# Kernel tuning notes

Measured on AMD Instinct MI355X. Metric: run time of the kernel, lower is better.

The kernel has to match this reference:

```python
import jax, jax.numpy as jnp
import numpy as np

N, D = 128, 512  # batch, hypercube dim (in_features == n_2d_layers == out_features)

def setup_inputs() -> dict:
    key = jax.random.key(0)
    k1, k2, k3 = jax.random.split(key, 3)
    bound = 1.0 / np.sqrt(D)
    x = jax.random.normal(k1, (N, D, D), dtype=jnp.float32)
    # kaiming_uniform_(a=sqrt(5)) on (in, layers, out) ~ U(-1/sqrt(fan_in), 1/sqrt(fan_in)) scale
    w = jax.random.uniform(k2, (D, D, D), dtype=jnp.float32, minval=-bound, maxval=bound)
    b = jax.random.uniform(k3, (D, D), dtype=jnp.float32, minval=-bound, maxval=bound)
    return {"x": x, "w": w, "b": b}

def reference(x, w, b):
    # Original: (x.expand((L, *x.shape)).movedim(0,-2) * w).sum(-1) + b
    # which reduces to out[n,i,j] = sum_k x[n,i,k] * w[i,j,k] + b[i,j]
    # (w axes: (in_features, n_2d_layers, out_features), all equal D)
    return jnp.einsum('nik,ijk->nij', x, w) + b
```

## Files before the change

kernel.cpp:

```cpp
#include <hip/hip_runtime.h>


#define Dd 512
#define DD (512 * 512)

typedef __attribute__((ext_vector_type(8))) short bf16x8;
typedef __attribute__((ext_vector_type(4))) short bf16x4;
typedef __attribute__((ext_vector_type(4))) float f32x4;

__device__ __forceinline__ short f2bf(float f) {
    unsigned u = __builtin_bit_cast(unsigned, f);
    u += 0x7FFFu + ((u >> 16) & 1u);
    return (short)(u >> 16);
}

__device__ __forceinline__ void glds16(const float* g, float* l) {
    __builtin_amdgcn_global_load_lds(
        (const __attribute__((address_space(1))) void*)g,
        (__attribute__((address_space(3))) void*)l, 16, 0, 0);
}

__global__ __launch_bounds__(512, 4)
void linear3d_kernel(const float* __restrict__ x,
                     const float* __restrict__ w,
                     const float* __restrict__ b,
                     float* __restrict__ out) {
    const int i    = blockIdx.x;
    const int tid  = threadIdx.x;
    const int lane = tid & 63;
    const int wid  = tid >> 6;
    const int row16 = lane & 15;
    const int cg    = lane >> 4;

    __shared__ float f32r[2][8192];
    __shared__ short b16s[8192];

    const float* xi = x + (size_t)i * Dd;
    const float* wi = w + (size_t)i * DD;

    #pragma unroll
    for (int q = 0; q < 4; ++q) { int t = wid * 4 + q;
        glds16(wi + t * 256 + lane * 4, &f32r[0][t * 256]); }
    #pragma unroll
    for (int q = 0; q < 4; ++q) { int t = wid * 4 + q;
        glds16(wi + 8192 + t * 256 + lane * 4, &f32r[1][t * 256]); }

    bf16x8 xf[16];
    for (int r = 0; r < 8; ++r) {
        __syncthreads();
        #pragma unroll
        for (int p = 0; p < 4; ++p) {
            int idx4 = tid + p * 512;
            int row = idx4 >> 7, c4 = idx4 & 127;
            float4 v = *(const float4*)(xi + (size_t)(r * 16 + row) * DD + c4 * 4);
            bf16x4 h = { f2bf(v.x), f2bf(v.y), f2bf(v.z), f2bf(v.w) };
            int byte = (row * 1024 + c4 * 8) ^ ((row & 7) << 4);
            *(bf16x4*)((char*)b16s + byte) = h;
        }
        __syncthreads();
        if (wid == r) {
            #pragma unroll
            for (int s = 0; s < 16; ++s) {
                int byte = (row16 * 1024 + s * 64 + cg * 16) ^ ((row16 & 7) << 4);
                xf[s] = *(const bf16x8*)((const char*)b16s + byte);
            }
        }
    }
    __syncthreads();

#define CVTW(V, q) do {                                                        \
    int row_  = 2 * wid + ((q) >> 1);                                          \
    int byte_ = (row_ * 1024 + ((q) & 1) * 512 + lane * 8) ^ ((row_ & 7) << 4);\
    bf16x4 h_ = { f2bf(V.x), f2bf(V.y), f2bf(V.z), f2bf(V.w) };                \
    *(bf16x4*)((char*)b16s + byte_) = h_;                                      \
} while (0)

    {
        asm volatile("s_waitcnt vmcnt(5)" ::: "memory");
        __builtin_amdgcn_sched_barrier(0);
        float4 v0 = *(const float4*)(&f32r[0][wid * 1024 +   0 + lane * 4]);
        float4 v1 = *(const float4*)(&f32r[0][wid * 1024 + 256 + lane * 4]);
        float4 v2 = *(const float4*)(&f32r[0][wid * 1024 + 512 + lane * 4]);
        float4 v3 = *(const float4*)(&f32r[0][wid * 1024 + 768 + lane * 4]);
        asm volatile("s_waitcnt lgkmcnt(0)" ::: "memory");
        __builtin_amdgcn_sched_barrier(0);
        #pragma unroll
        for (int q = 0; q < 4; ++q) { int t = wid * 4 + q;
            glds16(wi + 2 * 8192 + t * 256 + lane * 4, &f32r[0][t * 256]); }
        CVTW(v0, 0); CVTW(v1, 1); CVTW(v2, 2); CVTW(v3, 3);
    }
    float bias = b[i * Dd + row16];
    asm volatile("s_waitcnt lgkmcnt(0)" ::: "memory");
    __builtin_amdgcn_s_barrier();

#define CHUNK_BODY(c, VMSTR, DO_GLDS, DO_CONV) do {                            \
    f32x4 accA = {0.f, 0.f, 0.f, 0.f}, accB = {0.f, 0.f, 0.f, 0.f};           \
    _Pragma("unroll")                                                          \
    for (int s = 0; s < 16; s += 2) {                                          \
        int byA = (row16 * 1024 + s * 64 + cg * 16) ^ ((row16 & 7) << 4);      \
        int byB = (row16 * 1024 + (s + 1) * 64 + cg * 16) ^ ((row16 & 7) << 4);\
        bf16x8 wfA = *(const bf16x8*)((const char*)b16s + byA);                \
        bf16x8 wfB = *(const bf16x8*)((const char*)b16s + byB);                \
        accA = __builtin_amdgcn_mfma_f32_16x16x32_bf16(xf[s], wfA, accA, 0, 0, 0);     \
        accB = __builtin_amdgcn_mfma_f32_16x16x32_bf16(xf[s + 1], wfB, accB, 0, 0, 0); \
    }                                                                          \
    { int j = (c) * 16 + row16;                                                \
      _Pragma("unroll")                                                        \
      for (int r_ = 0; r_ < 4; ++r_) {                                         \
          int n_ = wid * 16 + cg * 4 + r_;                                     \
          out[(size_t)i * Dd + (size_t)n_ * DD + j] = accA[r_] + accB[r_] + bias; \
      } }                                                                      \
    asm volatile("s_waitcnt lgkmcnt(0)" ::: "memory");                         \
    __builtin_amdgcn_s_barrier();                                              \
    if (DO_CONV) {                                                             \
        const float* fb = &f32r[((c) + 1) & 1][0];                             \
        asm volatile("s_waitcnt " VMSTR ::: "memory");                         \
        __builtin_amdgcn_sched_barrier(0);                                     \
        float4 v0 = *(const float4*)(fb + wid * 1024 +   0 + lane * 4);        \
        float4 v1 = *(const float4*)(fb + wid * 1024 + 256 + lane * 4);        \
        float4 v2 = *(const float4*)(fb + wid * 1024 + 512 + lane * 4);        \
        float4 v3 = *(const float4*)(fb + wid * 1024 + 768 + lane * 4);        \
        asm volatile("s_waitcnt lgkmcnt(0)" ::: "memory");                     \
        __builtin_amdgcn_sched_barrier(0);                                     \
        if (DO_GLDS) {                                                         \
            const float* gs = wi + (size_t)((c) + 3) * 8192;                   \
            float* lb = &f32r[((c) + 1) & 1][0];                               \
            _Pragma("unroll")                                                  \
            for (int q = 0; q < 4; ++q) { int t = wid * 4 + q;                 \
                glds16(gs + t * 256 + lane * 4, lb + t * 256); }               \
        }                                                                      \
        bias = b[i * Dd + ((c) + 1) * 16 + row16];                             \
        CVTW(v0, 0); CVTW(v1, 1); CVTW(v2, 2); CVTW(v3, 3);                    \
        asm volatile("s_waitcnt lgkmcnt(0)" ::: "memory");                     \
        __builtin_amdgcn_s_barrier();                                          \
    }                                                                          \
} while (0)

    CHUNK_BODY(0, "vmcnt(9)", true, true);
    for (int c = 1; c <= 29; ++c)
        CHUNK_BODY(c, "vmcnt(14)", (c + 3 < 32), true);
    CHUNK_BODY(30, "vmcnt(10)", false, true);
    CHUNK_BODY(31, "vmcnt(0)", false, false);

#undef CHUNK_BODY
#undef CVTW
}

extern "C" void kernel_launch(void* const* d_in, const int* in_sizes, int n_in,
                              void* d_out, int out_size, void* d_ws, size_t ws_size,
                              hipStream_t stream) {
    const float* x = (const float*)d_in[0];
    const float* w = (const float*)d_in[1];
    const float* b = (const float*)d_in[2];
    float* out = (float*)d_out;
    linear3d_kernel<<<dim3(Dd), dim3(512), 0, stream>>>(x, w, b, out);
}
```

Measured before the change: 205.6 us.

## Load x fragments directly to registers and restructure W prefetch pipeline

Replaces the staged x-to-LDS path, which used 8 rounds with two block barriers each, with direct per-lane global loads of the x row fragments, software-pipelined and converted to bf16 in registers. The W chunk prefetch moves to the start of each chunk body so it overlaps the MFMA work, and the bias load is hoisted ahead of the compute. Barrier placement inside the chunk is reorganised and the vmcnt thresholds are retuned to match. The main loop is marked not-unrolled. This removes LDS traffic and synchronisation in the prologue, at the cost of strided uncoalesced x loads and a riskier wait-count scheme.

```diff
diff --git a/kernel.cpp b/kernel.cpp
--- a/kernel.cpp
+++ b/kernel.cpp
@@ -12,6 +12,13 @@
     unsigned u = __builtin_bit_cast(unsigned, f);
     u += 0x7FFFu + ((u >> 16) & 1u);
     return (short)(u >> 16);
+}
+
+__device__ __forceinline__ bf16x8 cvt8(float4 a, float4 b) {
+    bf16x8 h;
+    h[0] = f2bf(a.x); h[1] = f2bf(a.y); h[2] = f2bf(a.z); h[3] = f2bf(a.w);
+    h[4] = f2bf(b.x); h[5] = f2bf(b.y); h[6] = f2bf(b.z); h[7] = f2bf(b.w);
+    return h;
 }
 
 __device__ __forceinline__ void glds16(const float* g, float* l) {
@@ -38,36 +45,6 @@
     const float* xi = x + (size_t)i * Dd;
     const float* wi = w + (size_t)i * DD;
 
-    #pragma unroll
-    for (int q = 0; q < 4; ++q) { int t = wid * 4 + q;
-        glds16(wi + t * 256 + lane * 4, &f32r[0][t * 256]); }
-    #pragma unroll
-    for (int q = 0; q < 4; ++q) { int t = wid * 4 + q;
-        glds16(wi + 8192 + t * 256 + lane * 4, &f32r[1][t * 256]); }
-
-    bf16x8 xf[16];
-    for (int r = 0; r < 8; ++r) {
-        __syncthreads();
-        #pragma unroll
-        for (int p = 0; p < 4; ++p) {
-            int idx4 = tid + p * 512;
-            int row = idx4 >> 7, c4 = idx4 & 127;
-            float4 v = *(const float4*)(xi + (size_t)(r * 16 + row) * DD + c4 * 4);
-            bf16x4 h = { f2bf(v.x), f2bf(v.y), f2bf(v.z), f2bf(v.w) };
-            int byte = (row * 1024 + c4 * 8) ^ ((row & 7) << 4);
-            *(bf16x4*)((char*)b16s + byte) = h;
-        }
-        __syncthreads();
-        if (wid == r) {
-            #pragma unroll
-            for (int s = 0; s < 16; ++s) {
-                int byte = (row16 * 1024 + s * 64 + cg * 16) ^ ((row16 & 7) << 4);
-                xf[s] = *(const bf16x8*)((const char*)b16s + byte);
-            }
-        }
-    }
-    __syncthreads();
-
 #define CVTW(V, q) do {                                                        \
     int row_  = 2 * wid + ((q) >> 1);                                          \
     int byte_ = (row_ * 1024 + ((q) & 1) * 512 + lane * 8) ^ ((row_ & 7) << 4);\
@@ -75,74 +52,111 @@
     *(bf16x4*)((char*)b16s + byte_) = h_;                                      \
 } while (0)
 
+    float bias_cur = b[i * Dd + row16];
+    #pragma unroll
+    for (int q = 0; q < 4; ++q) { int t = wid * 4 + q;
+        glds16(wi + t * 256 + lane * 4, &f32r[0][t * 256]); }
+    #pragma unroll
+    for (int q = 0; q < 4; ++q) { int t = wid * 4 + q;
+        glds16(wi + 8192 + t * 256 + lane * 4, &f32r[1][t * 256]); }
+    asm volatile("" ::: "memory");
+
+    const float* xrow = xi + (size_t)(wid * 16 + row16) * DD + cg * 8;
+    float4 pa0 = *(const float4*)(xrow + 0);
+    float4 pa1 = *(const float4*)(xrow + 4);
+    float4 pa2 = *(const float4*)(xrow + 32);
+    float4 pa3 = *(const float4*)(xrow + 36);
+
+    asm volatile("s_waitcnt vmcnt(8)" ::: "memory");
+    __builtin_amdgcn_sched_barrier(0);
     {
-        asm volatile("s_waitcnt vmcnt(5)" ::: "memory");
-        __builtin_amdgcn_sched_barrier(0);
         float4 v0 = *(const float4*)(&f32r[0][wid * 1024 +   0 + lane * 4]);
         float4 v1 = *(const float4*)(&f32r[0][wid * 1024 + 256 + lane * 4]);
         float4 v2 = *(const float4*)(&f32r[0][wid * 1024 + 512 + lane * 4]);
         float4 v3 = *(const float4*)(&f32r[0][wid * 1024 + 768 + lane * 4]);
-        asm volatile("s_waitcnt lgkmcnt(0)" ::: "memory");
-        __builtin_amdgcn_sched_barrier(0);
-        #pragma unroll
-        for (int q = 0; q < 4; ++q) { int t = wid * 4 + q;
-            glds16(wi + 2 * 8192 + t * 256 + lane * 4, &f32r[0][t * 256]); }
         CVTW(v0, 0); CVTW(v1, 1); CVTW(v2, 2); CVTW(v3, 3);
     }
-    float bias = b[i * Dd + row16];
+
+    bf16x8 xf[16];
+    #pragma unroll
+    for (int r = 0; r < 8; ++r) {
+        float4 pb0, pb1, pb2, pb3;
+        if (r < 7) {
+            const float* xb = xrow + (2 * r + 2) * 32;
+            pb0 = *(const float4*)(xb + 0);
+            pb1 = *(const float4*)(xb + 4);
+            pb2 = *(const float4*)(xb + 32);
+            pb3 = *(const float4*)(xb + 36);
+        }
+        if (r < 7) asm volatile("s_waitcnt vmcnt(4)" ::: "memory");
+        else       asm volatile("s_waitcnt vmcnt(0)" ::: "memory");
+        __builtin_amdgcn_sched_barrier(0);
+        xf[2 * r]     = cvt8(pa0, pa1);
+        xf[2 * r + 1] = cvt8(pa2, pa3);
+        pa0 = pb0; pa1 = pb1; pa2 = pb2; pa3 = pb3;
+    }
+
     asm volatile("s_waitcnt lgkmcnt(0)" ::: "memory");
+    #pragma unroll
+    for (int q = 0; q < 4; ++q) { int t = wid * 4 + q;
+        glds16(wi + 2 * 8192 + t * 256 + lane * 4, &f32r[0][t * 256]); }
     __builtin_amdgcn_s_barrier();
+    __builtin_amdgcn_sched_barrier(0);
 
-#define CHUNK_BODY(c, VMSTR, DO_GLDS, DO_CONV) do {                            \
-    f32x4 accA = {0.f, 0.f, 0.f, 0.f}, accB = {0.f, 0.f, 0.f, 0.f};           \
+#define BODY(c, VMSTR, DO_GLDS, DO_CONV, DO_BIAS) do {                         \
+    if (DO_GLDS) {                                                             \
+        const float* gs_ = wi + (size_t)((c) + 2) * 8192;                      \
+        float* lb_ = &f32r[(c) & 1][0];                                        \
+        _Pragma("unroll")                                                      \
+        for (int q = 0; q < 4; ++q) { int t_ = wid * 4 + q;                    \
+            glds16(gs_ + t_ * 256 + lane * 4, lb_ + t_ * 256); }               \
+    }                                                                          \
+    float biasN_ = bias_cur;                                                   \
+    if (DO_BIAS) biasN_ = b[i * Dd + ((c) + 1) * 16 + row16];                  \
+    f32x4 accA = {0.f, 0.f, 0.f, 0.f}, accB = {0.f, 0.f, 0.f, 0.f};            \
     _Pragma("unroll")                                                          \
     for (int s = 0; s < 16; s += 2) {                                          \
-        int byA = (row16 * 1024 + s * 64 + cg * 16) ^ ((row16 & 7) << 4);      \
-        int byB = (row16 * 1024 + (s + 1) * 64 + cg * 16) ^ ((row16 & 7) << 4);\
-        bf16x8 wfA = *(const bf16x8*)((const char*)b16s + byA);                \
-        bf16x8 wfB = *(const bf16x8*)((const char*)b16s + byB);                \
-        accA = __builtin_amdgcn_mfma_f32_16x16x32_bf16(xf[s], wfA, accA, 0, 0, 0);     \
-        accB = __builtin_amdgcn_mfma_f32_16x16x32_bf16(xf[s + 1], wfB, accB, 0, 0, 0); \
+        int byA_ = (row16 * 1024 + s * 64 + cg * 16) ^ ((row16 & 7) << 4);     \
+        int byB_ = (row16 * 1024 + (s + 1) * 64 + cg * 16) ^ ((row16 & 7) << 4);\
+        bf16x8 wfA_ = *(const bf16x8*)((const char*)b16s + byA_);              \
+        bf16x8 wfB_ = *(const bf16x8*)((const char*)b16s + byB_);              \
+        accA = __builtin_amdgcn_mfma_f32_16x16x32_bf16(xf[s], wfA_, accA, 0, 0, 0);       \
+        accB = __builtin_amdgcn_mfma_f32_16x16x32_bf16(xf[s + 1], wfB_, accB, 0, 0, 0);   \
     }                                                                          \
-    { int j = (c) * 16 + row16;                                                \
+    { int j_ = (c) * 16 + row16;                                               \
       _Pragma("unroll")                                                        \
       for (int r_ = 0; r_ < 4; ++r_) {                                         \
           int n_ = wid * 16 + cg * 4 + r_;                                     \
-          out[(size_t)i * Dd + (size_t)n_ * DD + j] = accA[r_] + accB[r_] + bias; \
+          out[(size_t)i * Dd + (size_t)n_ * DD + j_] =                         \
+              accA[r_] + accB[r_] + bias_cur;                                  \
       } }                                                                      \
-    asm volatile("s_waitcnt lgkmcnt(0)" ::: "memory");                         \
-    __builtin_amdgcn_s_barrier();                                              \
     if (DO_CONV) {                                                             \
-        const float* fb = &f32r[((c) + 1) & 1][0];                             \
         asm volatile("s_waitcnt " VMSTR ::: "memory");                         \
         __builtin_amdgcn_sched_barrier(0);                                     \
-        float4 v0 = *(const float4*)(fb + wid * 1024 +   0 + lane * 4);        \
-        float4 v1 = *(const float4*)(fb + wid * 1024 + 256 + lane * 4);        \
-        float4 v2 = *(const float4*)(fb + wid * 1024 + 512 + lane * 4);        \
-        float4 v3 = *(const float4*)(fb + wid * 1024 + 768 + lane * 4);        \
+        const float* fb_ = &f32r[((c) + 1) & 1][0];                            \
+        float4 v0_ = *(const float4*)(fb_ + wid * 1024 +   0 + lane * 4);      \
+        float4 v1_ = *(const float4*)(fb_ + wid * 1024 + 256 + lane * 4);      \
+        float4 v2_ = *(const float4*)(fb_ + wid * 1024 + 512 + lane * 4);      \
+        float4 v3_ = *(const float4*)(fb_ + wid * 1024 + 768 + lane * 4);      \
+        asm volatile("" ::: "memory");                                         \
+        __builtin_amdgcn_s_barrier();     \
+        __builtin_amdgcn_sched_barrier(0);                                     \
+        CVTW(v0_, 0); CVTW(v1_, 1); CVTW(v2_, 2); CVTW(v3_, 3);                \
         asm volatile("s_waitcnt lgkmcnt(0)" ::: "memory");                     \
+        __builtin_amdgcn_s_barrier();                \
         __builtin_amdgcn_sched_barrier(0);                                     \
-        if (DO_GLDS) {                                                         \
-            const float* gs = wi + (size_t)((c) + 3) * 8192;                   \
-            float* lb = &f32r[((c) + 1) & 1][0];                               \
-            _Pragma("unroll")                                                  \
-            for (int q = 0; q < 4; ++q) { int t = wid * 4 + q;                 \
-                glds16(gs + t * 256 + lane * 4, lb + t * 256); }               \
-        }                                                                      \
-        bias = b[i * Dd + ((c) + 1) * 16 + row16];                             \
-        CVTW(v0, 0); CVTW(v1, 1); CVTW(v2, 2); CVTW(v3, 3);                    \
-        asm volatile("s_waitcnt lgkmcnt(0)" ::: "memory");                     \
-        __builtin_amdgcn_s_barrier();                                          \
     }                                                                          \
+    bias_cur = biasN_;                                                         \
 } while (0)
 
-    CHUNK_BODY(0, "vmcnt(9)", true, true);
+    BODY(0, "vmcnt(9)", false, true, true);
+    #pragma unroll 1
     for (int c = 1; c <= 29; ++c)
-        CHUNK_BODY(c, "vmcnt(14)", (c + 3 < 32), true);
-    CHUNK_BODY(30, "vmcnt(10)", false, true);
-    CHUNK_BODY(31, "vmcnt(0)", false, false);
+        BODY(c, "vmcnt(13)", true, true, true);
+    BODY(30, "vmcnt(9)", false, true, true);
+    BODY(31, "vmcnt(0)", false, false, false);
 
-#undef CHUNK_BODY
+#undef BODY
 #undef CVTW
 }
 
```

Result: slower. 218.0 us (+6.0%).

## Convert W fp32 to bf16 in-register from swizzled LDS, dropping bf16 staging buffer

Applied to the files above, without the earlier changes.

Removes the separate bf16 LDS staging pass for W. The fp32 W tiles are now loaded into LDS with a swizzled layout and converted to bf16 right before each MFMA. This drops one LDS write/read round-trip and one barrier per chunk, and reuses the second fp32 buffer for the initial x staging. The cost is that each wave repeats the conversion on every read, there is more LDS read traffic because fp32 is read instead of bf16, and the prefetch pipeline is shallower (two buffers, one barrier).

```diff
diff --git a/kernel.cpp b/kernel.cpp
--- a/kernel.cpp
+++ b/kernel.cpp
@@ -12,6 +12,13 @@
     unsigned u = __builtin_bit_cast(unsigned, f);
     u += 0x7FFFu + ((u >> 16) & 1u);
     return (short)(u >> 16);
+}
+
+__device__ __forceinline__ bf16x8 cvt8(float4 a, float4 b) {
+    bf16x8 h;
+    h[0] = f2bf(a.x); h[1] = f2bf(a.y); h[2] = f2bf(a.z); h[3] = f2bf(a.w);
+    h[4] = f2bf(b.x); h[5] = f2bf(b.y); h[6] = f2bf(b.z); h[7] = f2bf(b.w);
+    return h;
 }
 
 __device__ __forceinline__ void glds16(const float* g, float* l) {
@@ -31,20 +38,26 @@
     const int wid  = tid >> 6;
     const int row16 = lane & 15;
     const int cg    = lane >> 4;
+    const int sw    = (row16 & 7) << 4;
 
     __shared__ float f32r[2][8192];
-    __shared__ short b16s[8192];
 
     const float* xi = x + (size_t)i * Dd;
     const float* wi = w + (size_t)i * DD;
 
-    #pragma unroll
-    for (int q = 0; q < 4; ++q) { int t = wid * 4 + q;
-        glds16(wi + t * 256 + lane * 4, &f32r[0][t * 256]); }
-    #pragma unroll
-    for (int q = 0; q < 4; ++q) { int t = wid * 4 + q;
-        glds16(wi + 8192 + t * 256 + lane * 4, &f32r[1][t * 256]); }
+#define WGLDS(cidx, slot) do {                                                 \
+    const float* gsrc_ = wi + (size_t)(cidx) * 8192;                           \
+    _Pragma("unroll")                                                          \
+    for (int q = 0; q < 4; ++q) {                                              \
+        int t_ = wid * 4 + q; int row_ = t_ >> 1;                              \
+        int off_ = (((t_ & 1) * 1024) + lane * 16) ^ ((row_ & 7) << 4);        \
+        glds16(gsrc_ + row_ * 512 + (off_ >> 2), &f32r[slot][t_ * 256]);       \
+    }                                                                          \
+} while (0)
 
+    WGLDS(0, 0);
+
+    short* xs = (short*)&f32r[1][0];
     bf16x8 xf[16];
     for (int r = 0; r < 8; ++r) {
         __syncthreads();
@@ -55,95 +68,68 @@
             float4 v = *(const float4*)(xi + (size_t)(r * 16 + row) * DD + c4 * 4);
             bf16x4 h = { f2bf(v.x), f2bf(v.y), f2bf(v.z), f2bf(v.w) };
             int byte = (row * 1024 + c4 * 8) ^ ((row & 7) << 4);
-            *(bf16x4*)((char*)b16s + byte) = h;
+            *(bf16x4*)((char*)xs + byte) = h;
         }
         __syncthreads();
         if (wid == r) {
             #pragma unroll
             for (int s = 0; s < 16; ++s) {
-                int byte = (row16 * 1024 + s * 64 + cg * 16) ^ ((row16 & 7) << 4);
-                xf[s] = *(const bf16x8*)((const char*)b16s + byte);
+                int byte = (row16 * 1024 + s * 64 + cg * 16) ^ sw;
+                xf[s] = *(const bf16x8*)((const char*)xs + byte);
             }
         }
     }
     __syncthreads();
 
-#define CVTW(V, q) do {                                                        \
-    int row_  = 2 * wid + ((q) >> 1);                                          \
-    int byte_ = (row_ * 1024 + ((q) & 1) * 512 + lane * 8) ^ ((row_ & 7) << 4);\
-    bf16x4 h_ = { f2bf(V.x), f2bf(V.y), f2bf(V.z), f2bf(V.w) };                \
-    *(bf16x4*)((char*)b16s + byte_) = h_;                                      \
-} while (0)
+    WGLDS(1, 1);
+    float bias_cur = b[i * Dd + row16];
 
-    {
-        asm volatile("s_waitcnt vmcnt(5)" ::: "memory");
-        __builtin_amdgcn_sched_barrier(0);
-        float4 v0 = *(const float4*)(&f32r[0][wid * 1024 +   0 + lane * 4]);
-        float4 v1 = *(const float4*)(&f32r[0][wid * 1024 + 256 + lane * 4]);
-        float4 v2 = *(const float4*)(&f32r[0][wid * 1024 + 512 + lane * 4]);
-        float4 v3 = *(const float4*)(&f32r[0][wid * 1024 + 768 + lane * 4]);
-        asm volatile("s_waitcnt lgkmcnt(0)" ::: "memory");
-        __builtin_amdgcn_sched_barrier(0);
-        #pragma unroll
-        for (int q = 0; q < 4; ++q) { int t = wid * 4 + q;
-            glds16(wi + 2 * 8192 + t * 256 + lane * 4, &f32r[0][t * 256]); }
-        CVTW(v0, 0); CVTW(v1, 1); CVTW(v2, 2); CVTW(v3, 3);
-    }
-    float bias = b[i * Dd + row16];
-    asm volatile("s_waitcnt lgkmcnt(0)" ::: "memory");
-    __builtin_amdgcn_s_barrier();
-
-#define CHUNK_BODY(c, VMSTR, DO_GLDS, DO_CONV) do {                            \
-    f32x4 accA = {0.f, 0.f, 0.f, 0.f}, accB = {0.f, 0.f, 0.f, 0.f};           \
+#define BODY(c, VMSTR, DO_GLDS, DO_BIAS, DO_SYNC) do {                         \
+    float biasN_ = bias_cur;                                                   \
+    if (DO_BIAS) biasN_ = b[i * Dd + ((c) + 1) * 16 + row16];                  \
+    const float* buf_ = &f32r[(c) & 1][0] + row16 * 512;                       \
+    const int K0_ = ((cg * 32) ^ sw) >> 2;                                     \
+    const int K1_ = ((cg * 32) ^ sw ^ 16) >> 2;                                \
+    f32x4 accA = {0.f, 0.f, 0.f, 0.f}, accB = {0.f, 0.f, 0.f, 0.f};            \
     _Pragma("unroll")                                                          \
     for (int s = 0; s < 16; s += 2) {                                          \
-        int byA = (row16 * 1024 + s * 64 + cg * 16) ^ ((row16 & 7) << 4);      \
-        int byB = (row16 * 1024 + (s + 1) * 64 + cg * 16) ^ ((row16 & 7) << 4);\
-        bf16x8 wfA = *(const bf16x8*)((const char*)b16s + byA);                \
-        bf16x8 wfB = *(const bf16x8*)((const char*)b16s + byB);                \
-        accA = __builtin_amdgcn_mfma_f32_16x16x32_bf16(xf[s], wfA, accA, 0, 0, 0);     \
-        accB = __builtin_amdgcn_mfma_f32_16x16x32_bf16(xf[s + 1], wfB, accB, 0, 0, 0); \
+        float4 a0_ = *(const float4*)(buf_ + K0_ + s * 32);                    \
+        float4 a1_ = *(const float4*)(buf_ + K1_ + s * 32);                    \
+        float4 b0_ = *(const float4*)(buf_ + K0_ + (s + 1) * 32);              \
+        float4 b1_ = *(const float4*)(buf_ + K1_ + (s + 1) * 32);              \
+        accA = __builtin_amdgcn_mfma_f32_16x16x32_bf16(                        \
+            xf[s], cvt8(a0_, a1_), accA, 0, 0, 0);                             \
+        accB = __builtin_amdgcn_mfma_f32_16x16x32_bf16(                        \
+            xf[s + 1], cvt8(b0_, b1_), accB, 0, 0, 0);                         \
     }                                                                          \
-    { int j = (c) * 16 + row16;                                                \
+    { int j_ = (c) * 16 + row16;                                               \
       _Pragma("unroll")                                                        \
       for (int r_ = 0; r_ < 4; ++r_) {                                         \
           int n_ = wid * 16 + cg * 4 + r_;                                     \
-          out[(size_t)i * Dd + (size_t)n_ * DD + j] = accA[r_] + accB[r_] + bias; \
+          out[(size_t)n_ * DD + (size_t)i * Dd + j_] =                         \
+              accA[r_] + accB[r_] + bias_cur;                                  \
       } }                                                                      \
-    asm volatile("s_waitcnt lgkmcnt(0)" ::: "memory");                         \
-    __builtin_amdgcn_s_barrier();                                              \
-    if (DO_CONV) {                                                             \
-        const float* fb = &f32r[((c) + 1) & 1][0];                             \
+    bias_cur = biasN_;                                                         \
+    if (DO_SYNC) {                                                             \
         asm volatile("s_waitcnt " VMSTR ::: "memory");                         \
+        __builtin_amdgcn_s_barrier();                                          \
         __builtin_amdgcn_sched_barrier(0);                                     \
-        float4 v0 = *(const float4*)(fb + wid * 1024 +   0 + lane * 4);        \
-        float4 v1 = *(const float4*)(fb + wid * 1024 + 256 + lane * 4);        \
-        float4 v2 = *(const float4*)(fb + wid * 1024 + 512 + lane * 4);        \
-        float4 v3 = *(const float4*)(fb + wid * 1024 + 768 + lane * 4);        \
-        asm volatile("s_waitcnt lgkmcnt(0)" ::: "memory");                     \
+    }                                                                          \
+    if (DO_GLDS) {                                                             \
+        WGLDS((c) + 2, (c) & 1);                                               \
         __builtin_amdgcn_sched_barrier(0);                                     \
-        if (DO_GLDS) {                                                         \
-            const float* gs = wi + (size_t)((c) + 3) * 8192;                   \
-            float* lb = &f32r[((c) + 1) & 1][0];                               \
-            _Pragma("unroll")                                                  \
-            for (int q = 0; q < 4; ++q) { int t = wid * 4 + q;                 \
-                glds16(gs + t * 256 + lane * 4, lb + t * 256); }               \
-        }                                                                      \
-        bias = b[i * Dd + ((c) + 1) * 16 + row16];                             \
-        CVTW(v0, 0); CVTW(v1, 1); CVTW(v2, 2); CVTW(v3, 3);                    \
-        asm volatile("s_waitcnt lgkmcnt(0)" ::: "memory");                     \
-        __builtin_amdgcn_s_barrier();                                          \
     }                                                                          \
 } while (0)
 
-    CHUNK_BODY(0, "vmcnt(9)", true, true);
+    BODY(0, "vmcnt(5)", true, true, true);
+    #pragma unroll 1
     for (int c = 1; c <= 29; ++c)
-        CHUNK_BODY(c, "vmcnt(14)", (c + 3 < 32), true);
-    CHUNK_BODY(30, "vmcnt(10)", false, true);
-    CHUNK_BODY(31, "vmcnt(0)", false, false);
+        BODY(c, "vmcnt(5)", true, true, true);
+    BODY(30, "vmcnt(5)", false, true, true);
+    BODY(31, "vmcnt(0)", false, false, false);
 
-#undef CHUNK_BODY
-#undef CVTW
+#undef BODY
+#undef WGLDS
 }
 
 extern "C" void kernel_launch(void* const* d_in, const int* in_sizes, int n_in,
```

New measurement: 190.1 us. -7.6%, faster.
